# Kernel optimization log

Hardware: AMD Instinct MI355X
Metric: run time of the kernel (lower is better)

Reference implementation:

```python
import math
import jax, jax.numpy as jnp
import numpy as np

NUM_BUCKETS = 32
MAX_DISTANCE = 128
N_HEADS = 16
D_KV = 64


def _relative_position_bucket(relative_position, num_buckets=NUM_BUCKETS, max_distance=MAX_DISTANCE):
    # bidirectional variant (encoder): half the buckets for each sign
    nb = num_buckets // 2
    n = -relative_position
    ret = (n < 0).astype(jnp.int32) * nb
    n = jnp.abs(n)
    max_exact = nb // 2
    is_small = n < max_exact
    val_if_large = max_exact + (
        jnp.log(jnp.maximum(n, 1).astype(jnp.float32) / max_exact)
        / math.log(max_distance / max_exact)
        * (nb - max_exact)
    ).astype(jnp.int32)
    val_if_large = jnp.minimum(val_if_large, nb - 1)
    return ret + jnp.where(is_small, n, val_if_large)


def setup_inputs() -> dict:
    key = jax.random.key(0)
    ks = jax.random.split(key, 6)
    d_model = 1024
    inner = N_HEADS * D_KV
    scale = 1.0 / math.sqrt(d_model)
    x = jax.random.normal(ks[0], (2, 2048, d_model), dtype=jnp.float32)
    wq = jax.random.normal(ks[1], (d_model, inner), dtype=jnp.float32) * scale
    wk = jax.random.normal(ks[2], (d_model, inner), dtype=jnp.float32) * scale
    wv = jax.random.normal(ks[3], (d_model, inner), dtype=jnp.float32) * scale
    wo = jax.random.normal(ks[4], (inner, d_model), dtype=jnp.float32) * scale
    rel_emb = jax.random.normal(ks[5], (NUM_BUCKETS, N_HEADS), dtype=jnp.float32)
    return {"x": x, "wq": wq, "wk": wk, "wv": wv, "wo": wo, "rel_emb": rel_emb}


def reference(x, wq, wk, wv, wo, rel_emb):
    B, S, D = x.shape
    # QKV projections (no bias, T5 style), split heads -> [B, S, H, Dk]
    q = (x @ wq).reshape(B, S, N_HEADS, D_KV)
    k = (x @ wk).reshape(B, S, N_HEADS, D_KV)
    v = (x @ wv).reshape(B, S, N_HEADS, D_KV)
    # NOTE: T5 does NOT scale by 1/sqrt(d_kv)
    scores = jnp.einsum("bqhd,bkhd->bhqk", q, k)  # [B, H, S, S]
    # relative position bias
    ctx = jnp.arange(S)[:, None]
    mem = jnp.arange(S)[None, :]
    buckets = _relative_position_bucket(mem - ctx)  # [S, S]
    bias = rel_emb[buckets]  # [S, S, H]
    bias = jnp.transpose(bias, (2, 0, 1))[None]  # [1, H, S, S]
    scores = scores + bias
    weights = jax.nn.softmax(scores.astype(jnp.float32), axis=-1).astype(scores.dtype)
    context = jnp.einsum("bhqk,bkhd->bqhd", weights, v).reshape(B, S, N_HEADS * D_KV)
    return context @ wo
```

## Files before the change

kernel.cpp:

```cpp
#include <hip/hip_runtime.h>
#include <hip/hip_bf16.h>

typedef __attribute__((ext_vector_type(8))) _Float16 f16x8;
typedef __attribute__((ext_vector_type(4))) float f32x4;
typedef unsigned short u16;
typedef unsigned int u32;

#define S_LEN 2048
#define NH    16
#define DK    64
#define DMODEL 1024
#define LSTR  40

union F16U { _Float16 h; u16 u; };
__device__ __forceinline__ u16 f2h(float f) {
    F16U v; v.h = (_Float16)f; return v.u;
}

__global__ __launch_bounds__(256) void bias_table_kernel(
    const float* __restrict__ rel_emb, float* __restrict__ tab)
{
    int idx = blockIdx.x * 256 + threadIdx.x;
    int h = idx >> 12;
    int t = idx & 4095;
    int rp = t - 2048;
    int n = -rp;
    int ret = 0;
    if (n < 0) { ret = 16; n = -n; }
    int inner;
    if (n < 8) {
        inner = n;
    } else {
        inner = 8 + (n >= 12) + (n >= 16) + (n >= 23) + (n >= 32)
                  + (n >= 46) + (n >= 64) + (n >= 91);
        if (inner > 15) inner = 15;
    }
    tab[h * 4096 + t] = rel_emb[(ret + inner) * NH + h];
}

__global__ __launch_bounds__(256) void convert_x(
    const float* __restrict__ X, u16* __restrict__ Xf)
{
    long i8 = ((long)blockIdx.x * 256 + threadIdx.x) * 8;
    float4 a = *(const float4*)&X[i8];
    float4 b = *(const float4*)&X[i8 + 4];
    *(ushort4*)&Xf[i8] =
        make_ushort4(f2h(a.x), f2h(a.y), f2h(a.z), f2h(a.w));
    *(ushort4*)&Xf[i8 + 4] =
        make_ushort4(f2h(b.x), f2h(b.y), f2h(b.z), f2h(b.w));
}

__global__ __launch_bounds__(256) void convert_wT(
    const float* __restrict__ Wq, const float* __restrict__ Wk,
    const float* __restrict__ Wv, const float* __restrict__ Wo,
    u16* __restrict__ WT)
{
    const float* src = (blockIdx.z == 0) ? Wq : (blockIdx.z == 1) ? Wk
                     : (blockIdx.z == 2) ? Wv : Wo;
    u16* dT = WT + (long)blockIdx.z * 1048576;
    __shared__ __align__(16) float T[64 * 68];
    const int k0 = blockIdx.y * 64, n0 = blockIdx.x * 64;
    const int tid = threadIdx.x;
    #pragma unroll
    for (int u = 0; u < 4; u++) {
        int w = tid + u * 256;
        int r = w >> 4, c4 = (w & 15) * 4;
        *(float4*)&T[r * 68 + c4] =
            *(const float4*)&src[(long)(k0 + r) * DMODEL + n0 + c4];
    }
    __syncthreads();
    #pragma unroll
    for (int u = 0; u < 4; u++) {
        int w = tid + u * 256;
        int n = w >> 4, kc = (w & 15) * 4;
        *(ushort4*)&dT[(long)(n0 + n) * DMODEL + k0 + kc] = make_ushort4(
            f2h(T[(kc + 0) * 68 + n]), f2h(T[(kc + 1) * 68 + n]),
            f2h(T[(kc + 2) * 68 + n]), f2h(T[(kc + 3) * 68 + n]));
    }
}

__global__ __launch_bounds__(256, 3) void gemm_qkv_mfma(
    const u16* __restrict__ Xf, const u16* __restrict__ WT,
    u16* __restrict__ Qf, u16* __restrict__ Kf, u16* __restrict__ VT)
{
    const int z = blockIdx.z;
    const u16* BT = WT + (long)z * 1048576;

    __shared__ __align__(16) u16 Ah[128 * LSTR], Bh[128 * LSTR];

    const int tid = threadIdx.x;
    const int wv = tid >> 6, lane = tid & 63;
    const int g = lane >> 4, li = lane & 15;
    const int wr = wv >> 1, wc = wv & 1;
    const int bm = blockIdx.y * 128, bn = blockIdx.x * 128;

    f32x4 acc[4][4];
    #pragma unroll
    for (int i = 0; i < 4; i++)
        #pragma unroll
        for (int j = 0; j < 4; j++) acc[i][j] = (f32x4){0.f, 0.f, 0.f, 0.f};

    for (int k0 = 0; k0 < DMODEL; k0 += 32) {
        #pragma unroll
        for (int u = 0; u < 2; u++) {
            int w = tid + u * 256;
            int row = w >> 2, q8 = (w & 3) * 8;
            *(uint4*)&Ah[row * LSTR + q8] =
                *(const uint4*)&Xf[(long)(bm + row) * DMODEL + k0 + q8];
            *(uint4*)&Bh[row * LSTR + q8] =
                *(const uint4*)&BT[(long)(bn + row) * DMODEL + k0 + q8];
        }
        __syncthreads();

        f16x8 a_h[4], b_h[4];
        #pragma unroll
        for (int i = 0; i < 4; i++)
            a_h[i] = *(const f16x8*)&Ah[(wr * 64 + i * 16 + li) * LSTR + g * 8];
        #pragma unroll
        for (int j = 0; j < 4; j++)
            b_h[j] = *(const f16x8*)&Bh[(wc * 64 + j * 16 + li) * LSTR + g * 8];
        #pragma unroll
        for (int i = 0; i < 4; i++)
            #pragma unroll
            for (int j = 0; j < 4; j++)
                acc[i][j] = __builtin_amdgcn_mfma_f32_16x16x32_f16(
                    a_h[i], b_h[j], acc[i][j], 0, 0, 0);
        __syncthreads();
    }

    if (z == 2) {
        #pragma unroll
        for (int i = 0; i < 4; i++) {
            int s_base = bm + wr * 64 + i * 16 + g * 4;
            int bb = s_base >> 11, s = s_base & 2047;
            #pragma unroll
            for (int j = 0; j < 4; j++) {
                int gcol = bn + wc * 64 + j * 16 + li;
                int hh = gcol >> 6, d = gcol & 63;
                long idx = (((long)(bb * NH + hh)) * DK + d) * S_LEN + s;
                *(ushort4*)&VT[idx] = make_ushort4(
                    f2h(acc[i][j][0]), f2h(acc[i][j][1]),
                    f2h(acc[i][j][2]), f2h(acc[i][j][3]));
            }
        }
    } else {
        u16* O = (z == 0) ? Qf : Kf;
        #pragma unroll
        for (int i = 0; i < 4; i++) {
            #pragma unroll
            for (int r = 0; r < 4; r++) {
                int grow = bm + wr * 64 + i * 16 + g * 4 + r;
                int bb = grow >> 11, s = grow & 2047;
                #pragma unroll
                for (int j = 0; j < 4; j++) {
                    int gcol = bn + wc * 64 + j * 16 + li;
                    int hh = gcol >> 6, d = gcol & 63;
                    long idx = (((long)(bb * NH + hh)) * S_LEN + s) * DK + d;
                    O[idx] = f2h(acc[i][j][r]);
                }
            }
        }
    }
}

__global__ __launch_bounds__(256, 3) void gemm_out_mfma(
    const u16* __restrict__ Ab, const u16* __restrict__ WT,
    float* __restrict__ O)
{
    const u16* BT = WT + 3L * 1048576;
    __shared__ __align__(16) u16 Ah[128 * LSTR], Bh[128 * LSTR];

    const int tid = threadIdx.x;
    const int wv = tid >> 6, lane = tid & 63;
    const int g = lane >> 4, li = lane & 15;
    const int wr = wv >> 1, wc = wv & 1;
    const int bm = blockIdx.y * 128, bn = blockIdx.x * 128;

    f32x4 acc[4][4];
    #pragma unroll
    for (int i = 0; i < 4; i++)
        #pragma unroll
        for (int j = 0; j < 4; j++) acc[i][j] = (f32x4){0.f, 0.f, 0.f, 0.f};

    for (int k0 = 0; k0 < DMODEL; k0 += 32) {
        #pragma unroll
        for (int u = 0; u < 2; u++) {
            int w = tid + u * 256;
            int row = w >> 2, q8 = (w & 3) * 8;
            *(uint4*)&Ah[row * LSTR + q8] =
                *(const uint4*)&Ab[(long)(bm + row) * DMODEL + k0 + q8];
            *(uint4*)&Bh[row * LSTR + q8] =
                *(const uint4*)&BT[(long)(bn + row) * DMODEL + k0 + q8];
        }
        __syncthreads();

        f16x8 a_h[4], b_h[4];
        #pragma unroll
        for (int i = 0; i < 4; i++)
            a_h[i] = *(const f16x8*)&Ah[(wr * 64 + i * 16 + li) * LSTR + g * 8];
        #pragma unroll
        for (int j = 0; j < 4; j++)
            b_h[j] = *(const f16x8*)&Bh[(wc * 64 + j * 16 + li) * LSTR + g * 8];
        #pragma unroll
        for (int i = 0; i < 4; i++)
            #pragma unroll
            for (int j = 0; j < 4; j++)
                acc[i][j] = __builtin_amdgcn_mfma_f32_16x16x32_f16(
                    a_h[i], b_h[j], acc[i][j], 0, 0, 0);
        __syncthreads();
    }

    #pragma unroll
    for (int i = 0; i < 4; i++)
        #pragma unroll
        for (int r = 0; r < 4; r++) {
            int grow = bm + wr * 64 + i * 16 + g * 4 + r;
            #pragma unroll
            for (int j = 0; j < 4; j++) {
                int gcol = bn + wc * 64 + j * 16 + li;
                O[(long)grow * DMODEL + gcol] = acc[i][j][r];
            }
        }
}

#define APAD 72

__global__ __launch_bounds__(256, 5) void attn_mfma(
    const u16* __restrict__ Qf, const u16* __restrict__ Kf,
    const u16* __restrict__ VT, const float* __restrict__ tab,
    u16* __restrict__ ctxb)
{
    __shared__ __align__(16) u16 Ks[64 * APAD];
    __shared__ __align__(16) u16 Vs[64 * APAD];
    __shared__ __align__(16) u16 Ps[64 * APAD];
    __shared__ float biasS[128];

    const int tid = threadIdx.x;
    const int wv = tid >> 6, lane = tid & 63;
    const int g = lane >> 4, li = lane & 15;
    const int qblk = blockIdx.x & 31;
    const int h = (blockIdx.x >> 5) & 15;
    const int b = blockIdx.x >> 9;
    const int q0 = qblk * 64;
    const long bh = b * NH + h;
    const int qloc = wv * 16 + li;

    const u16* KhG = Kf + bh * (S_LEN * DK);
    const u16* VtG = VT + bh * (DK * S_LEN);
    const float* th = tab + h * 4096;

    f16x8 q0f, q1f;
    {
        long qrow = bh * S_LEN + q0 + qloc;
        const u16* ph = Qf + qrow * DK + g * 8;
        q0f = *(const f16x8*)ph;  q1f = *(const f16x8*)(ph + 32);
    }

    f32x4 Oc[4];
    #pragma unroll
    for (int n = 0; n < 4; n++) Oc[n] = (f32x4){0.f, 0.f, 0.f, 0.f};
    float mP = -1e30f, lR = 0.f;

    for (int kt0 = 0; kt0 < S_LEN; kt0 += 64) {
        #pragma unroll
        for (int u = 0; u < 2; u++) {
            int w = tid + u * 256;
            int row = w >> 3, c8 = (w & 7) * 8;
            *(uint4*)&Ks[row * APAD + c8] =
                *(const uint4*)&KhG[(long)(kt0 + row) * DK + c8];
            *(uint4*)&Vs[row * APAD + c8] =
                *(const uint4*)&VtG[(long)row * S_LEN + kt0 + c8];
        }
        if (tid < 128) {
            int idx = kt0 + tid - 63 - q0 + 2048;
            idx = idx < 0 ? 0 : (idx > 4095 ? 4095 : idx);
            biasS[tid] = th[idx];
        }
        __syncthreads();

        f32x4 Sa[4];
        #pragma unroll
        for (int m = 0; m < 4; m++) {
            const u16* kp = &Ks[(m * 16 + li) * APAD + g * 8];
            f16x8 k0 = *(const f16x8*)kp, k1 = *(const f16x8*)(kp + 32);
            f32x4 s = (f32x4){0.f, 0.f, 0.f, 0.f};
            s = __builtin_amdgcn_mfma_f32_16x16x32_f16(k0, q0f, s, 0, 0, 0);
            s = __builtin_amdgcn_mfma_f32_16x16x32_f16(k1, q1f, s, 0, 0, 0);
            Sa[m] = s;
        }

        #pragma unroll
        for (int m = 0; m < 4; m++)
            #pragma unroll
            for (int r = 0; r < 4; r++)
                Sa[m][r] += biasS[m * 16 + g * 4 + r + 63 - qloc];

        float pm = Sa[0][0];
        #pragma unroll
        for (int m = 0; m < 4; m++)
            #pragma unroll
            for (int r = 0; r < 4; r++) pm = fmaxf(pm, Sa[m][r]);
        pm = fmaxf(pm, __shfl_xor(pm, 16));
        pm = fmaxf(pm, __shfl_xor(pm, 32));

        float mn = fmaxf(mP, pm);
        float alpha = __expf(mP - mn);
        mP = mn;

        float ls = 0.f;
        #pragma unroll
        for (int m = 0; m < 4; m++)
            #pragma unroll
            for (int r = 0; r < 4; r++) {
                Sa[m][r] = __expf(Sa[m][r] - mn);
                ls += Sa[m][r];
            }
        ls += __shfl_xor(ls, 16);
        ls += __shfl_xor(ls, 32);
        lR = lR * alpha + ls;

        float aO[4];
        #pragma unroll
        for (int r = 0; r < 4; r++) aO[r] = __shfl(alpha, g * 4 + r);
        #pragma unroll
        for (int n = 0; n < 4; n++)
            #pragma unroll
            for (int r = 0; r < 4; r++) Oc[n][r] *= aO[r];

        #pragma unroll
        for (int m = 0; m < 4; m++)
            *(ushort4*)&Ps[qloc * APAD + m * 16 + g * 4] = make_ushort4(
                f2h(Sa[m][0]), f2h(Sa[m][1]), f2h(Sa[m][2]), f2h(Sa[m][3]));

        {
            const u16* pp = &Ps[qloc * APAD + g * 8];
            f16x8 p0 = *(const f16x8*)pp, p1 = *(const f16x8*)(pp + 32);
            #pragma unroll
            for (int n = 0; n < 4; n++) {
                const u16* vp = &Vs[(n * 16 + li) * APAD + g * 8];
                f16x8 v0 = *(const f16x8*)vp, v1 = *(const f16x8*)(vp + 32);
                Oc[n] = __builtin_amdgcn_mfma_f32_16x16x32_f16(p0, v0, Oc[n], 0, 0, 0);
                Oc[n] = __builtin_amdgcn_mfma_f32_16x16x32_f16(p1, v1, Oc[n], 0, 0, 0);
            }
        }
        __syncthreads();
    }

    float linv = 1.0f / lR;
    float iv[4];
    #pragma unroll
    for (int r = 0; r < 4; r++) iv[r] = __shfl(linv, g * 4 + r);
    #pragma unroll
    for (int n = 0; n < 4; n++)
        #pragma unroll
        for (int r = 0; r < 4; r++)
            ctxb[((long)(b * S_LEN + q0 + wv * 16 + g * 4 + r)) * DMODEL
                 + h * DK + n * 16 + li] = f2h(Oc[n][r] * iv[r]);
}

extern "C" void kernel_launch(void* const* d_in, const int* in_sizes, int n_in,
                              void* d_out, int out_size, void* d_ws, size_t ws_size,
                              hipStream_t stream)
{
    const float* x    = (const float*)d_in[0];
    const float* wq   = (const float*)d_in[1];
    const float* wk   = (const float*)d_in[2];
    const float* wv   = (const float*)d_in[3];
    const float* wo   = (const float*)d_in[4];
    const float* rel  = (const float*)d_in[5];

    u16* W0 = (u16*)d_ws;
    u16* Xf  = W0;
    u16* Qf  = W0 + 4194304;
    u16* Kf  = W0 + 8388608;
    u16* VT  = W0 + 12582912;
    u16* WT  = W0 + 16777216;
    float* tab = (float*)(W0 + 20971520);
    u16* ctxb = Xf;

    bias_table_kernel<<<dim3(256), dim3(256), 0, stream>>>(rel, tab);
    convert_x<<<dim3(2048), dim3(256), 0, stream>>>(x, Xf);
    convert_wT<<<dim3(16, 16, 4), dim3(256), 0, stream>>>(wq, wk, wv, wo, WT);
    gemm_qkv_mfma<<<dim3(8, 32, 3), dim3(256), 0, stream>>>(Xf, WT, Qf, Kf, VT);
    attn_mfma<<<dim3(1024), dim3(256), 0, stream>>>(Qf, Kf, VT, tab, ctxb);
    gemm_out_mfma<<<dim3(8, 32), dim3(256), 0, stream>>>(ctxb, WT, (float*)d_out);
}
```

Measured before the change: 240.8 us.

## Prefetch next tiles into registers in GEMMs and attention, use exp2 softmax

Both GEMM kernels and the attention kernel now issue global loads for the next K-tile into registers before computing on the current tile, then store them to LDS between two barriers. This hides global-load latency behind the MFMA work. The attention softmax moves to base 2: the bias table is pre-scaled by log2(e) and scores are folded in with fmaf before exp2f. The rescale of the running max is skipped when no lane's max grew, and s_setprio brackets the MFMA sections. The attention occupancy hint drops from 5 to 4 blocks per SM to make room for the extra prefetch registers.

```diff
diff --git a/kernel.cpp b/kernel.cpp
--- a/kernel.cpp
+++ b/kernel.cpp
@@ -11,6 +11,7 @@
 #define DK    64
 #define DMODEL 1024
 #define LSTR  40
+#define LOG2E 1.44269504f
 
 union F16U { _Float16 h; u16 u; };
 __device__ __forceinline__ u16 f2h(float f) {
@@ -35,7 +36,7 @@
                   + (n >= 46) + (n >= 64) + (n >= 91);
         if (inner > 15) inner = 15;
     }
-    tab[h * 4096 + t] = rel_emb[(ret + inner) * NH + h];
+    tab[h * 4096 + t] = rel_emb[(ret + inner) * NH + h] * LOG2E;
 }
 
 __global__ __launch_bounds__(256) void convert_x(
@@ -94,23 +95,37 @@
     const int wr = wv >> 1, wc = wv & 1;
     const int bm = blockIdx.y * 128, bn = blockIdx.x * 128;
 
+    const int srow = tid >> 2, sq8 = (tid & 3) * 8;
+    const u16* As0 = &Xf[(long)(bm + srow) * DMODEL + sq8];
+    const u16* As1 = &Xf[(long)(bm + srow + 64) * DMODEL + sq8];
+    const u16* Bs0 = &BT[(long)(bn + srow) * DMODEL + sq8];
+    const u16* Bs1 = &BT[(long)(bn + srow + 64) * DMODEL + sq8];
+    u16* AL0 = &Ah[srow * LSTR + sq8];
+    u16* AL1 = &Ah[(srow + 64) * LSTR + sq8];
+    u16* BL0 = &Bh[srow * LSTR + sq8];
+    u16* BL1 = &Bh[(srow + 64) * LSTR + sq8];
+
     f32x4 acc[4][4];
     #pragma unroll
     for (int i = 0; i < 4; i++)
         #pragma unroll
         for (int j = 0; j < 4; j++) acc[i][j] = (f32x4){0.f, 0.f, 0.f, 0.f};
 
+    *(uint4*)AL0 = *(const uint4*)As0;
+    *(uint4*)AL1 = *(const uint4*)As1;
+    *(uint4*)BL0 = *(const uint4*)Bs0;
+    *(uint4*)BL1 = *(const uint4*)Bs1;
+    __syncthreads();
+
     for (int k0 = 0; k0 < DMODEL; k0 += 32) {
-        #pragma unroll
-        for (int u = 0; u < 2; u++) {
-            int w = tid + u * 256;
-            int row = w >> 2, q8 = (w & 3) * 8;
-            *(uint4*)&Ah[row * LSTR + q8] =
-                *(const uint4*)&Xf[(long)(bm + row) * DMODEL + k0 + q8];
-            *(uint4*)&Bh[row * LSTR + q8] =
-                *(const uint4*)&BT[(long)(bn + row) * DMODEL + k0 + q8];
-        }
-        __syncthreads();
+        const bool have = (k0 + 32) < DMODEL;
+        uint4 na0, na1, nb0, nb1;
+        if (have) {
+            na0 = *(const uint4*)(As0 + k0 + 32);
+            na1 = *(const uint4*)(As1 + k0 + 32);
+            nb0 = *(const uint4*)(Bs0 + k0 + 32);
+            nb1 = *(const uint4*)(Bs1 + k0 + 32);
+        }
 
         f16x8 a_h[4], b_h[4];
         #pragma unroll
@@ -125,7 +140,13 @@
             for (int j = 0; j < 4; j++)
                 acc[i][j] = __builtin_amdgcn_mfma_f32_16x16x32_f16(
                     a_h[i], b_h[j], acc[i][j], 0, 0, 0);
-        __syncthreads();
+
+        if (have) {
+            __syncthreads();
+            *(uint4*)AL0 = na0; *(uint4*)AL1 = na1;
+            *(uint4*)BL0 = nb0; *(uint4*)BL1 = nb1;
+            __syncthreads();
+        }
     }
 
     if (z == 2) {
@@ -176,23 +197,37 @@
     const int wr = wv >> 1, wc = wv & 1;
     const int bm = blockIdx.y * 128, bn = blockIdx.x * 128;
 
+    const int srow = tid >> 2, sq8 = (tid & 3) * 8;
+    const u16* As0 = &Ab[(long)(bm + srow) * DMODEL + sq8];
+    const u16* As1 = &Ab[(long)(bm + srow + 64) * DMODEL + sq8];
+    const u16* Bs0 = &BT[(long)(bn + srow) * DMODEL + sq8];
+    const u16* Bs1 = &BT[(long)(bn + srow + 64) * DMODEL + sq8];
+    u16* AL0 = &Ah[srow * LSTR + sq8];
+    u16* AL1 = &Ah[(srow + 64) * LSTR + sq8];
+    u16* BL0 = &Bh[srow * LSTR + sq8];
+    u16* BL1 = &Bh[(srow + 64) * LSTR + sq8];
+
     f32x4 acc[4][4];
     #pragma unroll
     for (int i = 0; i < 4; i++)
         #pragma unroll
         for (int j = 0; j < 4; j++) acc[i][j] = (f32x4){0.f, 0.f, 0.f, 0.f};
 
+    *(uint4*)AL0 = *(const uint4*)As0;
+    *(uint4*)AL1 = *(const uint4*)As1;
+    *(uint4*)BL0 = *(const uint4*)Bs0;
+    *(uint4*)BL1 = *(const uint4*)Bs1;
+    __syncthreads();
+
     for (int k0 = 0; k0 < DMODEL; k0 += 32) {
-        #pragma unroll
-        for (int u = 0; u < 2; u++) {
-            int w = tid + u * 256;
-            int row = w >> 2, q8 = (w & 3) * 8;
-            *(uint4*)&Ah[row * LSTR + q8] =
-                *(const uint4*)&Ab[(long)(bm + row) * DMODEL + k0 + q8];
-            *(uint4*)&Bh[row * LSTR + q8] =
-                *(const uint4*)&BT[(long)(bn + row) * DMODEL + k0 + q8];
-        }
-        __syncthreads();
+        const bool have = (k0 + 32) < DMODEL;
+        uint4 na0, na1, nb0, nb1;
+        if (have) {
+            na0 = *(const uint4*)(As0 + k0 + 32);
+            na1 = *(const uint4*)(As1 + k0 + 32);
+            nb0 = *(const uint4*)(Bs0 + k0 + 32);
+            nb1 = *(const uint4*)(Bs1 + k0 + 32);
+        }
 
         f16x8 a_h[4], b_h[4];
         #pragma unroll
@@ -207,7 +242,13 @@
             for (int j = 0; j < 4; j++)
                 acc[i][j] = __builtin_amdgcn_mfma_f32_16x16x32_f16(
                     a_h[i], b_h[j], acc[i][j], 0, 0, 0);
-        __syncthreads();
+
+        if (have) {
+            __syncthreads();
+            *(uint4*)AL0 = na0; *(uint4*)AL1 = na1;
+            *(uint4*)BL0 = nb0; *(uint4*)BL1 = nb1;
+            __syncthreads();
+        }
     }
 
     #pragma unroll
@@ -225,7 +266,7 @@
 
 #define APAD 72
 
-__global__ __launch_bounds__(256, 5) void attn_mfma(
+__global__ __launch_bounds__(256, 4) void attn_mfma(
     const u16* __restrict__ Qf, const u16* __restrict__ Kf,
     const u16* __restrict__ VT, const float* __restrict__ tab,
     u16* __restrict__ ctxb)
@@ -249,6 +290,8 @@
     const u16* VtG = VT + bh * (DK * S_LEN);
     const float* th = tab + h * 4096;
 
+    const int srow = tid >> 3, sc8 = (tid & 7) * 8;
+
     f16x8 q0f, q1f;
     {
         long qrow = bh * S_LEN + q0 + qloc;
@@ -256,29 +299,45 @@
         q0f = *(const f16x8*)ph;  q1f = *(const f16x8*)(ph + 32);
     }
 
+    *(uint4*)&Ks[srow * APAD + sc8] =
+        *(const uint4*)&KhG[(long)srow * DK + sc8];
+    *(uint4*)&Ks[(srow + 32) * APAD + sc8] =
+        *(const uint4*)&KhG[(long)(srow + 32) * DK + sc8];
+    *(uint4*)&Vs[srow * APAD + sc8] =
+        *(const uint4*)&VtG[(long)srow * S_LEN + sc8];
+    *(uint4*)&Vs[(srow + 32) * APAD + sc8] =
+        *(const uint4*)&VtG[(long)(srow + 32) * S_LEN + sc8];
+    if (tid < 128) {
+        int idx = tid - 63 - q0 + 2048;
+        idx = idx < 0 ? 0 : (idx > 4095 ? 4095 : idx);
+        biasS[tid] = th[idx];
+    }
+    __syncthreads();
+
     f32x4 Oc[4];
     #pragma unroll
     for (int n = 0; n < 4; n++) Oc[n] = (f32x4){0.f, 0.f, 0.f, 0.f};
     float mP = -1e30f, lR = 0.f;
 
     for (int kt0 = 0; kt0 < S_LEN; kt0 += 64) {
-        #pragma unroll
-        for (int u = 0; u < 2; u++) {
-            int w = tid + u * 256;
-            int row = w >> 3, c8 = (w & 7) * 8;
-            *(uint4*)&Ks[row * APAD + c8] =
-                *(const uint4*)&KhG[(long)(kt0 + row) * DK + c8];
-            *(uint4*)&Vs[row * APAD + c8] =
-                *(const uint4*)&VtG[(long)row * S_LEN + kt0 + c8];
-        }
-        if (tid < 128) {
-            int idx = kt0 + tid - 63 - q0 + 2048;
-            idx = idx < 0 ? 0 : (idx > 4095 ? 4095 : idx);
-            biasS[tid] = th[idx];
-        }
-        __syncthreads();
+        const int ktn = kt0 + 64;
+        const bool havenext = ktn < S_LEN;
+
+        uint4 nk0, nk1, nv0, nv1; float nb = 0.f;
+        if (havenext) {
+            nk0 = *(const uint4*)&KhG[(long)(ktn + srow) * DK + sc8];
+            nk1 = *(const uint4*)&KhG[(long)(ktn + srow + 32) * DK + sc8];
+            nv0 = *(const uint4*)&VtG[(long)srow * S_LEN + ktn + sc8];
+            nv1 = *(const uint4*)&VtG[(long)(srow + 32) * S_LEN + ktn + sc8];
+            if (tid < 128) {
+                int idx = ktn + tid - 63 - q0 + 2048;
+                idx = idx < 0 ? 0 : (idx > 4095 ? 4095 : idx);
+                nb = th[idx];
+            }
+        }
 
         f32x4 Sa[4];
+        __builtin_amdgcn_s_setprio(1);
         #pragma unroll
         for (int m = 0; m < 4; m++) {
             const u16* kp = &Ks[(m * 16 + li) * APAD + g * 8];
@@ -288,44 +347,50 @@
             s = __builtin_amdgcn_mfma_f32_16x16x32_f16(k1, q1f, s, 0, 0, 0);
             Sa[m] = s;
         }
+        __builtin_amdgcn_s_setprio(0);
 
         #pragma unroll
         for (int m = 0; m < 4; m++)
             #pragma unroll
             for (int r = 0; r < 4; r++)
-                Sa[m][r] += biasS[m * 16 + g * 4 + r + 63 - qloc];
-
-        float pm = Sa[0][0];
+                Sa[m][r] = fmaf(Sa[m][r], LOG2E,
+                                biasS[m * 16 + g * 4 + r + 63 - qloc]);
+
+        float mm[4];
         #pragma unroll
         for (int m = 0; m < 4; m++)
-            #pragma unroll
-            for (int r = 0; r < 4; r++) pm = fmaxf(pm, Sa[m][r]);
+            mm[m] = fmaxf(fmaxf(Sa[m][0], Sa[m][1]),
+                          fmaxf(Sa[m][2], Sa[m][3]));
+        float pm = fmaxf(fmaxf(mm[0], mm[1]), fmaxf(mm[2], mm[3]));
         pm = fmaxf(pm, __shfl_xor(pm, 16));
         pm = fmaxf(pm, __shfl_xor(pm, 32));
 
-        float mn = fmaxf(mP, pm);
-        float alpha = __expf(mP - mn);
-        mP = mn;
-
-        float ls = 0.f;
-        #pragma unroll
-        for (int m = 0; m < 4; m++)
-            #pragma unroll
-            for (int r = 0; r < 4; r++) {
-                Sa[m][r] = __expf(Sa[m][r] - mn);
-                ls += Sa[m][r];
-            }
+        if (__any(pm > mP)) {
+            float mn = fmaxf(mP, pm);
+            float alpha = __builtin_amdgcn_exp2f(mP - mn);
+            mP = mn;
+            lR *= alpha;
+            float aO[4];
+            #pragma unroll
+            for (int r = 0; r < 4; r++) aO[r] = __shfl(alpha, g * 4 + r);
+            #pragma unroll
+            for (int n = 0; n < 4; n++)
+                #pragma unroll
+                for (int r = 0; r < 4; r++) Oc[n][r] *= aO[r];
+        }
+
+        float sm[4];
+        #pragma unroll
+        for (int m = 0; m < 4; m++) {
+            #pragma unroll
+            for (int r = 0; r < 4; r++)
+                Sa[m][r] = __builtin_amdgcn_exp2f(Sa[m][r] - mP);
+            sm[m] = (Sa[m][0] + Sa[m][1]) + (Sa[m][2] + Sa[m][3]);
+        }
+        float ls = (sm[0] + sm[1]) + (sm[2] + sm[3]);
         ls += __shfl_xor(ls, 16);
         ls += __shfl_xor(ls, 32);
-        lR = lR * alpha + ls;
-
-        float aO[4];
-        #pragma unroll
-        for (int r = 0; r < 4; r++) aO[r] = __shfl(alpha, g * 4 + r);
-        #pragma unroll
-        for (int n = 0; n < 4; n++)
-            #pragma unroll
-            for (int r = 0; r < 4; r++) Oc[n][r] *= aO[r];
+        lR += ls;
 
         #pragma unroll
         for (int m = 0; m < 4; m++)
@@ -335,6 +400,7 @@
         {
             const u16* pp = &Ps[qloc * APAD + g * 8];
             f16x8 p0 = *(const f16x8*)pp, p1 = *(const f16x8*)(pp + 32);
+            __builtin_amdgcn_s_setprio(1);
             #pragma unroll
             for (int n = 0; n < 4; n++) {
                 const u16* vp = &Vs[(n * 16 + li) * APAD + g * 8];
@@ -342,8 +408,18 @@
                 Oc[n] = __builtin_amdgcn_mfma_f32_16x16x32_f16(p0, v0, Oc[n], 0, 0, 0);
                 Oc[n] = __builtin_amdgcn_mfma_f32_16x16x32_f16(p1, v1, Oc[n], 0, 0, 0);
             }
-        }
-        __syncthreads();
+            __builtin_amdgcn_s_setprio(0);
+        }
+
+        if (havenext) {
+            __syncthreads();
+            *(uint4*)&Ks[srow * APAD + sc8] = nk0;
+            *(uint4*)&Ks[(srow + 32) * APAD + sc8] = nk1;
+            *(uint4*)&Vs[srow * APAD + sc8] = nv0;
+            *(uint4*)&Vs[(srow + 32) * APAD + sc8] = nv1;
+            if (tid < 128) biasS[tid] = nb;
+            __syncthreads();
+        }
     }
 
     float linv = 1.0f / lR;
```

Measured after the change: 223.5 us. 1.08x faster.
